# Kernel optimization log

Measured on AMD Instinct MI355X. Metric: run time of the kernel, lower is better.

The kernel has to match this reference:

```python
import jax, jax.numpy as jnp
import numpy as np

HEADS = 5 - 1  # 4 attention heads (GPSConv heads=4)


def _bn(x, g, b, eps=1e-5):
    # BatchNorm1d, training-mode math (biased variance), matches torch normalization
    mu = x.mean(0)
    var = x.var(0)
    return g * (x - mu) * jax.lax.rsqrt(var + eps) + b


def _forward(x, t, freqs, t_fc1_W, t_fc1_b, t_fc2_W, t_fc2_b, node_W, node_b,
             tproj_W, tproj_b, tcat_W, tcat_b, pen_g, pen_b, pel_W, pel_b,
             cat_W, cat_b, conv_Wg, gru_Wih, gru_bih, gru_Whh, gru_bhh,
             attn_Wqkv, attn_bqkv, attn_Wo, attn_bo, bn_g, bn_b,
             mlp_W1, mlp_b1, mlp_W2, mlp_b2, out_W, out_b):
    B, C, Hh, Ww = x.shape
    HD = node_W.shape[1]          # hidden_dim = 64
    DH = HD // HEADS              # per-head dim = 16
    WL = pen_g.shape[0]           # walk_length = 20

    xf = x.reshape(B, -1)                              # [B, D]
    h = xf @ node_W + node_b                           # node_proj

    # TimeEmbedding: t @ freqs -> sin/cos -> MLP, then time_proj
    tp = t.reshape(B, 1) * freqs.reshape(1, -1)        # [B, nf]
    two_pi = jnp.asarray(2.0 * np.pi, x.dtype)
    te = jnp.concatenate([jnp.sin(two_pi * tp), jnp.cos(two_pi * tp)], axis=-1)
    te = jax.nn.silu(te @ t_fc1_W + t_fc1_b) @ t_fc2_W + t_fc2_b
    h_time = te @ tproj_W + tproj_b
    h = jnp.concatenate([h, h_time], axis=-1) @ tcat_W + tcat_b  # time_cat_proj

    # Fully-connected graph incl. self-loops: A = 1 everywhere, deg = B.
    # Random-walk PE: P = A/deg has all entries 1/B; P is idempotent (P@P = P),
    # hence diag(P^k) = diag(P) = 1/B for every k in 1..walk_length.
    A = jnp.ones((B, B), x.dtype)
    P = A / A.sum(1, keepdims=True)
    pe = jnp.broadcast_to(jnp.diagonal(P)[:, None], (B, WL))
    pe = _bn(pe, pen_g, pen_b)                         # pe_norm (batch stats)
    h = jnp.concatenate([h, pe @ pel_W + pel_b], axis=-1) @ cat_W + cat_b

    inv_sqrt = jnp.asarray(1.0 / np.sqrt(DH), x.dtype)
    for l in range(conv_Wg.shape[0]):                  # 5 GPSConv layers
        # --- GatedGraphConv (num_layers=1): message, add-aggregate, GRU ---
        m = A @ (h @ conv_Wg[l])                       # sum of messages from all src nodes
        gi = m @ gru_Wih[l] + gru_bih[l]               # [B, 3H]
        gh = h @ gru_Whh[l] + gru_bhh[l]
        ir, iz, inn = jnp.split(gi, 3, axis=-1)
        hr, hz, hn = jnp.split(gh, 3, axis=-1)
        r = jax.nn.sigmoid(ir + hr)
        z = jax.nn.sigmoid(iz + hz)
        n = jnp.tanh(inn + r * hn)
        hc = (1.0 - z) * n + z * h                     # GRUCell output
        h1 = _bn(hc + h, bn_g[l, 0], bn_b[l, 0])       # residual + norm1

        # --- global multihead self-attention over the single dense batch ---
        qkv = h @ attn_Wqkv[l] + attn_bqkv[l]
        q, k, v = jnp.split(qkv, 3, axis=-1)
        q = q.reshape(B, HEADS, DH).transpose(1, 0, 2)  # [h, B, d]
        k = k.reshape(B, HEADS, DH).transpose(1, 0, 2)
        v = v.reshape(B, HEADS, DH).transpose(1, 0, 2)
        att = jax.nn.softmax(jnp.einsum('hqd,hkd->hqk', q, k) * inv_sqrt, axis=-1)
        o = jnp.einsum('hqk,hkd->hqd', att, v).transpose(1, 0, 2).reshape(B, HD)
        o = o @ attn_Wo[l] + attn_bo[l]
        h2 = _bn(o + h, bn_g[l, 1], bn_b[l, 1])        # residual + norm2

        s = h1 + h2
        s = s + (jax.nn.relu(s @ mlp_W1[l] + mlp_b1[l]) @ mlp_W2[l] + mlp_b2[l])
        h = _bn(s, bn_g[l, 2], bn_b[l, 2])             # norm3

    return (h @ out_W + out_b).reshape(B, C, Hh, Ww)


def setup_inputs() -> dict:
    key = jax.random.key(0)
    B, C, H, W = 2048, 4, 32, 32
    D = C * H * W                 # 4096
    HD, PE, WL, L = 64, 16, 20, 5
    NF, TH, TC = 8, 64, 64
    ks = iter(jax.random.split(key, 40))

    def rn(shape, s=0.05):
        return jax.random.normal(next(ks), shape, jnp.float32) * s

    return {
        'x': jax.random.normal(next(ks), (B, C, H, W), jnp.float32),
        't': jax.random.uniform(next(ks), (B,), jnp.float32),
        'freqs': rn((NF,), 1.0),
        't_fc1_W': rn((2 * NF, TH)), 't_fc1_b': rn((TH,)),
        't_fc2_W': rn((TH, TC)), 't_fc2_b': rn((TC,)),
        'node_W': rn((D, HD), 0.02), 'node_b': rn((HD,)),
        'tproj_W': rn((TC, HD)), 'tproj_b': rn((HD,)),
        'tcat_W': rn((2 * HD, HD)), 'tcat_b': rn((HD,)),
        'pen_g': jnp.ones((WL,), jnp.float32), 'pen_b': jnp.zeros((WL,), jnp.float32),
        'pel_W': rn((WL, PE)), 'pel_b': rn((PE,)),
        'cat_W': rn((HD + PE, HD)), 'cat_b': rn((HD,)),
        'conv_Wg': rn((L, HD, HD)),
        'gru_Wih': rn((L, HD, 3 * HD)), 'gru_bih': rn((L, 3 * HD)),
        'gru_Whh': rn((L, HD, 3 * HD)), 'gru_bhh': rn((L, 3 * HD)),
        'attn_Wqkv': rn((L, HD, 3 * HD)), 'attn_bqkv': rn((L, 3 * HD)),
        'attn_Wo': rn((L, HD, HD)), 'attn_bo': rn((L, HD)),
        'bn_g': jnp.ones((L, 3, HD), jnp.float32), 'bn_b': jnp.zeros((L, 3, HD), jnp.float32),
        'mlp_W1': rn((L, HD, 2 * HD)), 'mlp_b1': rn((L, 2 * HD)),
        'mlp_W2': rn((L, 2 * HD, HD)), 'mlp_b2': rn((L, HD)),
        'out_W': rn((HD, D)), 'out_b': rn((D,)),
    }


def reference(x, t, freqs, t_fc1_W, t_fc1_b, t_fc2_W, t_fc2_b, node_W, node_b,
              tproj_W, tproj_b, tcat_W, tcat_b, pen_g, pen_b, pel_W, pel_b,
              cat_W, cat_b, conv_Wg, gru_Wih, gru_bih, gru_Whh, gru_bhh,
              attn_Wqkv, attn_bqkv, attn_Wo, attn_bo, bn_g, bn_b,
              mlp_W1, mlp_b1, mlp_W2, mlp_b2, out_W, out_b):
    return _forward(x, t, freqs, t_fc1_W, t_fc1_b, t_fc2_W, t_fc2_b, node_W, node_b,
                    tproj_W, tproj_b, tcat_W, tcat_b, pen_g, pen_b, pel_W, pel_b,
                    cat_W, cat_b, conv_Wg, gru_Wih, gru_bih, gru_Whh, gru_bhh,
                    attn_Wqkv, attn_bqkv, attn_Wo, attn_bo, bn_g, bn_b,
                    mlp_W1, mlp_b1, mlp_W2, mlp_b2, out_W, out_b)
```

## Files before the change

### kernel.cpp

```cpp
#include <hip/hip_runtime.h>

#define NB 2048
#define HDM 64
#define NLAY 5

typedef __bf16 bf16x8 __attribute__((ext_vector_type(8)));
typedef float v4f __attribute__((ext_vector_type(4)));

__device__ __forceinline__ float sigmoidf_(float x){ return 1.f/(1.f+__expf(-x)); }
__device__ __forceinline__ float tanhfast_(float x){
  x = fminf(fmaxf(x, -15.f), 15.f);
  float e = __expf(2.f*x);
  return (e-1.f)/(e+1.f);
}
__device__ __forceinline__ unsigned short f2b_rne(float f){
  unsigned u = __float_as_uint(f);
  unsigned r = u + 0x7FFFu + ((u>>16)&1u);
  return (unsigned short)(r>>16);
}
__device__ __forceinline__ unsigned pk2(float a, float b){
  unsigned ua = (__float_as_uint(a) + 0x8000u) >> 16;
  unsigned ub = (__float_as_uint(b) + 0x8000u) & 0xFFFF0000u;
  return ua | ub;
}

__global__ __launch_bounds__(256) void k_pre(
    const float* __restrict__ x, const float* __restrict__ tt,
    const float* __restrict__ freqs,
    const float* __restrict__ fc1W, const float* __restrict__ fc1b,
    const float* __restrict__ fc2W, const float* __restrict__ fc2b,
    const float* __restrict__ tprojW, const float* __restrict__ tprojb,
    const float* __restrict__ nodeW,
    float* __restrict__ h0p, float* __restrict__ htime,
    float* __restrict__ zero_region)
{
  __shared__ float xs[16*260];
  __shared__ float tb0[128];
  __shared__ float tb1[128];
  const int t = threadIdx.x, blk = blockIdx.x;
  const int r = t>>6, c = t&63;

  if (blk == 0){
    for (int i = t; i < 320 + 1920; i += 256) zero_region[i] = 0.f;
  }

  {
    const int row = blk*2 + (r&1);
    const float tv = tt[row];
    if (r < 2){
      float te[16];
      #pragma unroll
      for (int j=0;j<8;++j){
        float sv, cv;
        __sincosf(6.28318530717958647692f*tv*freqs[j], &sv, &cv);
        te[j]=sv; te[j+8]=cv;
      }
      float a = fc1b[c];
      #pragma unroll
      for (int j=0;j<16;++j) a += te[j]*fc1W[j*64+c];
      tb0[r*64+c] = a*sigmoidf_(a);
    }
    __syncthreads();
    if (r < 2){
      float b2 = fc2b[c];
      #pragma unroll 8
      for (int k=0;k<64;++k) b2 += tb0[r*64+k]*fc2W[k*64+c];
      tb1[r*64+c] = b2;
    }
    __syncthreads();
    if (r < 2){
      float hti = tprojb[c];
      #pragma unroll 8
      for (int k=0;k<64;++k) hti += tb1[r*64+k]*tprojW[k*64+c];
      htime[row*64+c] = hti;
    }
  }

  const int rg = blk>>3, kq = blk&7;
  const int rows0 = rg*16, k0 = kq*512;
  const int col4 = (t&15)*4;
  const int rq4  = ((t>>4)&3)*4;
  const int ksub = (t>>6)*64;

  float4 a0={0,0,0,0}, a1={0,0,0,0}, a2={0,0,0,0}, a3={0,0,0,0};

  for (int ch=0; ch<2; ++ch){
    __syncthreads();
    #pragma unroll
    for (int i=0;i<4;++i){
      int fi = t + 256*i;
      int xr = fi>>6, kk = (fi&63)<<2;
      *(float4*)&xs[xr*260+kk] = *(const float4*)&x[(size_t)(rows0+xr)*4096 + k0 + ch*256 + kk];
    }
    __syncthreads();
    const float* wp = &nodeW[(size_t)(k0 + ch*256 + ksub)*64 + col4];
    const float* xp = &xs[rq4*260 + ksub];
    #pragma unroll 8
    for (int kk=0; kk<64; ++kk){
      float4 w  = *(const float4*)&wp[kk*64];
      float x0 = xp[kk];
      float x1 = xp[260+kk];
      float x2 = xp[520+kk];
      float x3 = xp[780+kk];
      a0.x += x0*w.x; a0.y += x0*w.y; a0.z += x0*w.z; a0.w += x0*w.w;
      a1.x += x1*w.x; a1.y += x1*w.y; a1.z += x1*w.z; a1.w += x1*w.w;
      a2.x += x2*w.x; a2.y += x2*w.y; a2.z += x2*w.z; a2.w += x2*w.w;
      a3.x += x3*w.x; a3.y += x3*w.y; a3.z += x3*w.z; a3.w += x3*w.w;
    }
  }
  __syncthreads();
  {
    const int kqi = t>>6;
    *(float4*)&xs[(kqi*16 + rq4 + 0)*64 + col4] = a0;
    *(float4*)&xs[(kqi*16 + rq4 + 1)*64 + col4] = a1;
    *(float4*)&xs[(kqi*16 + rq4 + 2)*64 + col4] = a2;
    *(float4*)&xs[(kqi*16 + rq4 + 3)*64 + col4] = a3;
  }
  __syncthreads();
  {
    const int row = t>>4, c4 = (t&15)*4;
    float4 s = {0,0,0,0};
    #pragma unroll
    for (int q=0;q<4;++q){
      float4 v = *(const float4*)&xs[(q*16+row)*64 + c4];
      s.x+=v.x; s.y+=v.y; s.z+=v.z; s.w+=v.w;
    }
    *(float4*)&h0p[(size_t)kq*(NB*HDM) + (rows0+row)*64 + c4] = s;
  }
}

__global__ __launch_bounds__(256) void k_assemble(
    const float* __restrict__ h0p, const float* __restrict__ htime,
    const float* __restrict__ nodeb,
    const float* __restrict__ tcatW, const float* __restrict__ tcatb,
    const float* __restrict__ penb, const float* __restrict__ pelW,
    const float* __restrict__ pelb,
    const float* __restrict__ catW, const float* __restrict__ catb,
    float* __restrict__ hbuf)
{
  __shared__ float sa[256];
  __shared__ float sb[256];
  __shared__ float cvec[64];
  const int t = threadIdx.x, blk = blockIdx.x;
  const int r = t>>6, c = t&63;
  const int row = blk*4 + r;

  if (r==0){
    float pl[16];
    #pragma unroll
    for (int j=0;j<16;++j){
      float a = pelb[j];
      for (int w=0;w<20;++w) a += penb[w]*pelW[w*16+j];
      pl[j]=a;
    }
    float a = catb[c];
    #pragma unroll
    for (int j=0;j<16;++j) a += pl[j]*catW[(64+j)*64+c];
    cvec[c]=a;
  }
  float h0 = nodeb[c];
  #pragma unroll
  for (int q=0;q<8;++q) h0 += h0p[(size_t)q*(NB*HDM) + row*64 + c];
  sa[t] = h0;
  sb[t] = htime[row*64+c];
  __syncthreads();
  float a = tcatb[c];
  #pragma unroll 4
  for (int k=0;k<64;++k){
    a += sa[r*64+k]*tcatW[k*64+c];
    a += sb[r*64+k]*tcatW[(64+k)*64+c];
  }
  __syncthreads();
  sa[t] = a;
  __syncthreads();
  float hv = cvec[c];
  #pragma unroll 8
  for (int k=0;k<64;++k) hv += sa[r*64+k]*catW[k*64+c];
  hbuf[row*64+c] = hv;
}

__global__ __launch_bounds__(256) void k_A(
    const float* __restrict__ smlp,
    const float* __restrict__ bnaccPrev,
    const float* __restrict__ gPrev, const float* __restrict__ bPrev,
    float* __restrict__ hbuf, float* __restrict__ hsumL,
    const float* __restrict__ Whh, const float* __restrict__ bhh,
    const float* __restrict__ Wq,  const float* __restrict__ bq,
    float* __restrict__ gh,
    unsigned short* __restrict__ Qb, unsigned short* __restrict__ Kb,
    unsigned short* __restrict__ Vt, int first)
{
  __shared__ float sa[8*64];
  const int t = threadIdx.x, blk = blockIdx.x;
  const int row0 = blk*8;

  #pragma unroll
  for (int i=0;i<2;++i){
    int idx = t + 256*i;
    int rl = idx>>6, c = idx&63;
    int row = row0 + rl;
    float hv;
    if (first){
      hv = hbuf[row*64+c];
    } else {
      float mu = bnaccPrev[256+c]*(1.f/NB);
      float va = bnaccPrev[320+c]*(1.f/NB) - mu*mu;
      hv = gPrev[c]*(smlp[row*64+c]-mu)*rsqrtf(va+1e-5f)+bPrev[c];
      hbuf[row*64+c] = hv;
    }
    sa[idx] = hv;
  }
  __syncthreads();
  if (t<64){
    float s = 0.f;
    #pragma unroll
    for (int rl=0;rl<8;++rl) s += sa[rl*64+t];
    atomicAdd(&hsumL[t], s);
  }
  if (t < 192){
    const int cc = t;
    float ag[8], aq[8];
    float bh = bhh[cc], bq_ = bq[cc];
    #pragma unroll
    for (int rl=0;rl<8;++rl){ ag[rl]=bh; aq[rl]=bq_; }
    #pragma unroll 4
    for (int k=0;k<64;++k){
      float wh = Whh[k*192+cc];
      float wq = Wq [k*192+cc];
      #pragma unroll
      for (int rl=0;rl<8;++rl){
        float hk = sa[rl*64+k];
        ag[rl] += hk*wh;
        aq[rl] += hk*wq;
      }
    }
    #pragma unroll
    for (int rl=0;rl<8;++rl){
      int rw = row0 + rl;
      gh[(size_t)rw*192+cc] = ag[rl];
      float aqv = aq[rl];
      if (cc < 64){
        int hd = cc>>4, dh = cc&15;
        size_t base = ((size_t)(hd<<11) + rw)*32;
        Qb[base+dh] = f2b_rne(aqv*0.25f);
        Qb[base+16+dh] = 0;
      } else if (cc < 128){
        int c2 = cc-64, hd = c2>>4, dh = c2&15;
        size_t base = ((size_t)(hd<<11) + rw)*32;
        Kb[base+dh] = f2b_rne(aqv);
        Kb[base+16+dh] = 0;
      } else {
        int c2 = cc-128, hd = c2>>4, dh = c2&15;
        Vt[((size_t)(hd*16+dh))*2048 + rw] = f2b_rne(aqv);
      }
    }
  }
}

__global__ __launch_bounds__(256) void k_attn(
    const unsigned short* __restrict__ Qb, const unsigned short* __restrict__ Kb,
    const unsigned short* __restrict__ Vt,
    float* __restrict__ o_out)
{
  __shared__ unsigned short Pl[4*640];
  __shared__ float Os[4*272];
  __shared__ float ms[64], ls[64];
  const int t = threadIdx.x;
  const int w = t>>6, lane = t&63;
  const int q15 = lane & 15, quad = lane >> 4;
  const int b = blockIdx.x;
  const int qt = b & 127, head = b>>7;
  const int qrow = qt*16 + q15;
  const int key00 = w*512;
  unsigned short* Plw = &Pl[w*640];

  const bf16x8 qf = *(const bf16x8*)&Qb[(((size_t)(head<<11))+qrow)*32 + quad*8];
  const unsigned short* Kb_h = Kb + ((size_t)(head<<11))*32;
  const unsigned short* Vrow = Vt + ((size_t)(head*16+q15))*2048;

  v4f O = {0.f,0.f,0.f,0.f};
  float m = -1e30f, lsum = 0.f;

  bf16x8 kf0 = *(const bf16x8*)&Kb_h[(size_t)(key00 + q15)*32 + quad*8];
  bf16x8 kf1 = *(const bf16x8*)&Kb_h[(size_t)(key00 + 16 + q15)*32 + quad*8];
  bf16x8 vf  = *(const bf16x8*)&Vrow[key00 + quad*8];

  for (int c=0; c<16; ++c){
    bf16x8 nk0, nk1, nv;
    if (c < 15){
      int nk = key00 + (c+1)*32;
      nk0 = *(const bf16x8*)&Kb_h[(size_t)(nk + q15)*32 + quad*8];
      nk1 = *(const bf16x8*)&Kb_h[(size_t)(nk + 16 + q15)*32 + quad*8];
      nv  = *(const bf16x8*)&Vrow[nk + quad*8];
    }
    v4f z = {0.f,0.f,0.f,0.f};
    v4f s0 = __builtin_amdgcn_mfma_f32_16x16x32_bf16(kf0, qf, z, 0,0,0);
    v4f s1 = __builtin_amdgcn_mfma_f32_16x16x32_bf16(kf1, qf, z, 0,0,0);
    float cmax = fmaxf(fmaxf(fmaxf(s0[0],s0[1]),fmaxf(s0[2],s0[3])),
                       fmaxf(fmaxf(s1[0],s1[1]),fmaxf(s1[2],s1[3])));
    cmax = fmaxf(cmax, __shfl_xor(cmax,16,64));
    cmax = fmaxf(cmax, __shfl_xor(cmax,32,64));
    float mnew = fmaxf(m, cmax);
    float alpha = __expf(m - mnew);
    float p0=__expf(s0[0]-mnew), p1=__expf(s0[1]-mnew), p2=__expf(s0[2]-mnew), p3=__expf(s0[3]-mnew);
    float p4=__expf(s1[0]-mnew), p5=__expf(s1[1]-mnew), p6=__expf(s1[2]-mnew), p7=__expf(s1[3]-mnew);
    lsum = alpha*lsum + ((p0+p1)+(p2+p3)+((p4+p5)+(p6+p7)));
    m = mnew;
    O[0]*=alpha; O[1]*=alpha; O[2]*=alpha; O[3]*=alpha;
    *(uint2*)&Plw[q15*40 + quad*4]      = make_uint2(pk2(p0,p1), pk2(p2,p3));
    *(uint2*)&Plw[q15*40 + 16 + quad*4] = make_uint2(pk2(p4,p5), pk2(p6,p7));
    asm volatile("s_waitcnt lgkmcnt(0)" ::: "memory");
    bf16x8 pf = *(const bf16x8*)&Plw[q15*40 + quad*8];
    O = __builtin_amdgcn_mfma_f32_16x16x32_bf16(vf, pf, O, 0,0,0);
    kf0 = nk0; kf1 = nk1; vf = nv;
  }
  lsum += __shfl_xor(lsum,16,64);
  lsum += __shfl_xor(lsum,32,64);
  #pragma unroll
  for (int j=0;j<4;++j) Os[w*272 + q15*17 + quad*4 + j] = O[j];
  if (quad==0){ ms[w*16+q15]=m; ls[w*16+q15]=lsum; }
  __syncthreads();
  {
    const int dh = t&15, q = t>>4;
    float m0=ms[q], m1=ms[16+q], m2=ms[32+q], m3=ms[48+q];
    float mm = fmaxf(fmaxf(m0,m1),fmaxf(m2,m3));
    float a0=__expf(m0-mm), a1=__expf(m1-mm), a2=__expf(m2-mm), a3=__expf(m3-mm);
    float ll = a0*ls[q]+a1*ls[16+q]+a2*ls[32+q]+a3*ls[48+q];
    float oo = a0*Os[q*17+dh] + a1*Os[272+q*17+dh] + a2*Os[544+q*17+dh] + a3*Os[816+q*17+dh];
    o_out[(size_t)(qt*16+q)*64 + head*16 + dh] = oo / ll;
  }
}

__global__ __launch_bounds__(256) void k_B2(
    const float* __restrict__ hbuf, const float* __restrict__ gh,
    const float* __restrict__ hsumL, const float* __restrict__ o_out,
    const float* __restrict__ Wg,   const float* __restrict__ Wih,
    const float* __restrict__ bih,  const float* __restrict__ Wo,
    const float* __restrict__ bo,
    float* __restrict__ s1, float* __restrict__ s2, float* __restrict__ bnaccL)
{
  __shared__ float sa[8*64];
  __shared__ float os[8*64];
  __shared__ float smv_[64];
  __shared__ float sgi[192];
  __shared__ float Sb1[8*64];
  __shared__ float Sb2[8*64];
  const int t = threadIdx.x, blk = blockIdx.x;
  const int row0 = blk*8;

  if (t<64){
    float a=0.f;
    #pragma unroll 8
    for (int k=0;k<64;++k) a += hsumL[k]*Wg[k*64+t];
    smv_[t]=a;
  }
  #pragma unroll
  for (int i=0;i<2;++i){
    int idx = t + 256*i;
    int rl = idx>>6, c = idx&63;
    sa[idx] = hbuf[(size_t)(row0+rl)*64+c];
    os[idx] = o_out[(size_t)(row0+rl)*64+c];
  }
  __syncthreads();
  if (t<192){
    float a = bih[t];
    #pragma unroll 8
    for (int k=0;k<64;++k) a += smv_[k]*Wih[k*192+t];
    sgi[t]=a;
  }
  __syncthreads();

  const int c = t&63, rg = t>>6;
  float o2a = bo[c], o2b = bo[c];
  #pragma unroll 4
  for (int k=0;k<64;++k){
    float w = Wo[k*64+c];
    o2a += os[(rg*2  )*64+k]*w;
    o2b += os[(rg*2+1)*64+k]*w;
  }
  #pragma unroll
  for (int i=0;i<2;++i){
    int rl = rg*2 + i;
    int row = row0 + rl;
    float o2 = i ? o2b : o2a;
    float hv = sa[rl*64+c];
    float s2v = o2 + hv;
    float ir = sgi[c]      + gh[(size_t)row*192+c];
    float iz = sgi[64+c]   + gh[(size_t)row*192+64+c];
    float inn = sgi[128+c];
    float hn  = gh[(size_t)row*192+128+c];
    float rr_ = sigmoidf_(ir);
    float zz  = sigmoidf_(iz);
    float nn  = tanhfast_(inn + rr_*hn);
    float s1v = (1.f-zz)*nn + zz*hv + hv;
    s1[(size_t)row*64+c] = s1v;
    s2[(size_t)row*64+c] = s2v;
    Sb1[rl*64+c] = s1v;
    Sb2[rl*64+c] = s2v;
  }
  __syncthreads();
  if (t<64){
    float a=0.f,aq=0.f,b=0.f,bq2=0.f;
    #pragma unroll
    for (int rl=0;rl<8;++rl){
      float v1 = Sb1[rl*64+t], v2 = Sb2[rl*64+t];
      a+=v1; aq+=v1*v1; b+=v2; bq2+=v2*v2;
    }
    atomicAdd(&bnaccL[t],a);     atomicAdd(&bnaccL[64+t],aq);
    atomicAdd(&bnaccL[128+t],b); atomicAdd(&bnaccL[192+t],bq2);
  }
}

__global__ __launch_bounds__(256) void k_C(
    const float* __restrict__ s1, const float* __restrict__ s2,
    const float* __restrict__ bngL, const float* __restrict__ bnbL,
    const float* __restrict__ W1, const float* __restrict__ b1,
    const float* __restrict__ W2, const float* __restrict__ b2,
    float* __restrict__ smlp, float* __restrict__ bnaccL)
{
  __shared__ float sa[8*64];
  __shared__ float sh[8*128];
  __shared__ float S2[8*64];
  const int t = threadIdx.x, blk = blockIdx.x;
  const int row0 = blk*8;

  #pragma unroll
  for (int i=0;i<2;++i){
    int idx = t + 256*i;
    int rl = idx>>6, c = idx&63;
    int row = row0 + rl;
    float mu1 = bnaccL[c]*(1.f/NB);
    float va1 = bnaccL[64+c]*(1.f/NB) - mu1*mu1;
    float mu2 = bnaccL[128+c]*(1.f/NB);
    float va2 = bnaccL[192+c]*(1.f/NB) - mu2*mu2;
    float h1 = bngL[c]*(s1[(size_t)row*64+c]-mu1)*rsqrtf(va1+1e-5f)+bnbL[c];
    float h2 = bngL[64+c]*(s2[(size_t)row*64+c]-mu2)*rsqrtf(va2+1e-5f)+bnbL[64+c];
    sa[idx] = h1+h2;
  }
  __syncthreads();
  {
    const int hj = t&127, rgq = t>>7;
    float a0v=b1[hj], a1v=b1[hj], a2v=b1[hj], a3v=b1[hj];
    #pragma unroll 4
    for (int k=0;k<64;++k){
      float w = W1[k*128+hj];
      a0v += sa[(rgq*4  )*64+k]*w;
      a1v += sa[(rgq*4+1)*64+k]*w;
      a2v += sa[(rgq*4+2)*64+k]*w;
      a3v += sa[(rgq*4+3)*64+k]*w;
    }
    sh[(rgq*4  )*128+hj] = fmaxf(a0v,0.f);
    sh[(rgq*4+1)*128+hj] = fmaxf(a1v,0.f);
    sh[(rgq*4+2)*128+hj] = fmaxf(a2v,0.f);
    sh[(rgq*4+3)*128+hj] = fmaxf(a3v,0.f);
  }
  __syncthreads();
  {
    const int c = t&63, rg = t>>6;
    float moa = b2[c], mob = b2[c];
    #pragma unroll 4
    for (int k=0;k<128;++k){
      float w = W2[k*64+c];
      moa += sh[(rg*2  )*128+k]*w;
      mob += sh[(rg*2+1)*128+k]*w;
    }
    #pragma unroll
    for (int i=0;i<2;++i){
      int rl = rg*2+i;
      float smv2 = sa[rl*64+c] + (i ? mob : moa);
      smlp[(size_t)(row0+rl)*64+c] = smv2;
      S2[rl*64+c] = smv2;
    }
  }
  __syncthreads();
  if (t<64){
    float a=0.f,aq=0.f;
    #pragma unroll
    for (int rl=0;rl<8;++rl){ float v=S2[rl*64+t]; a+=v; aq+=v*v; }
    atomicAdd(&bnaccL[256+t],a); atomicAdd(&bnaccL[320+t],aq);
  }
}

__global__ __launch_bounds__(256) void k_out(
  const float* __restrict__ smlp, const float* __restrict__ bnacc4,
  const float* __restrict__ g4, const float* __restrict__ b4,
  const float* __restrict__ outW, const float* __restrict__ outb,
  float* __restrict__ out)
{
  __shared__ float hsT[64*20];
  const int t = threadIdx.x, blk = blockIdx.x;
  const int rg = blk>>2, cg = blk&3;
  const int rows0 = rg*16;
  #pragma unroll
  for (int i=0;i<4;++i){
    int idx = t + 256*i;
    int k = idx&63, rr = idx>>6;
    float mu = bnacc4[256+k]*(1.f/NB);
    float va = bnacc4[320+k]*(1.f/NB)-mu*mu;
    hsT[k*20+rr] = g4[k]*(smlp[(size_t)(rows0+rr)*64+k]-mu)*rsqrtf(va+1e-5f)+b4[k];
  }
  __syncthreads();
  const int cc = cg*1024 + t*4;
  float4 acc[16];
  {
    float4 bv = *(const float4*)&outb[cc];
    #pragma unroll
    for (int rr=0;rr<16;++rr) acc[rr]=bv;
  }
  #pragma unroll 4
  for (int k=0;k<64;++k){
    float4 w = *(const float4*)&outW[(size_t)k*4096+cc];
    const float4* hp = (const float4*)&hsT[k*20];
    float4 h0=hp[0], h1=hp[1], h2=hp[2], h3=hp[3];
    acc[0].x+=h0.x*w.x;  acc[0].y+=h0.x*w.y;  acc[0].z+=h0.x*w.z;  acc[0].w+=h0.x*w.w;
    acc[1].x+=h0.y*w.x;  acc[1].y+=h0.y*w.y;  acc[1].z+=h0.y*w.z;  acc[1].w+=h0.y*w.w;
    acc[2].x+=h0.z*w.x;  acc[2].y+=h0.z*w.y;  acc[2].z+=h0.z*w.z;  acc[2].w+=h0.z*w.w;
    acc[3].x+=h0.w*w.x;  acc[3].y+=h0.w*w.y;  acc[3].z+=h0.w*w.z;  acc[3].w+=h0.w*w.w;
    acc[4].x+=h1.x*w.x;  acc[4].y+=h1.x*w.y;  acc[4].z+=h1.x*w.z;  acc[4].w+=h1.x*w.w;
    acc[5].x+=h1.y*w.x;  acc[5].y+=h1.y*w.y;  acc[5].z+=h1.y*w.z;  acc[5].w+=h1.y*w.w;
    acc[6].x+=h1.z*w.x;  acc[6].y+=h1.z*w.y;  acc[6].z+=h1.z*w.z;  acc[6].w+=h1.z*w.w;
    acc[7].x+=h1.w*w.x;  acc[7].y+=h1.w*w.y;  acc[7].z+=h1.w*w.z;  acc[7].w+=h1.w*w.w;
    acc[8].x+=h2.x*w.x;  acc[8].y+=h2.x*w.y;  acc[8].z+=h2.x*w.z;  acc[8].w+=h2.x*w.w;
    acc[9].x+=h2.y*w.x;  acc[9].y+=h2.y*w.y;  acc[9].z+=h2.y*w.z;  acc[9].w+=h2.y*w.w;
    acc[10].x+=h2.z*w.x; acc[10].y+=h2.z*w.y; acc[10].z+=h2.z*w.z; acc[10].w+=h2.z*w.w;
    acc[11].x+=h2.w*w.x; acc[11].y+=h2.w*w.y; acc[11].z+=h2.w*w.z; acc[11].w+=h2.w*w.w;
    acc[12].x+=h3.x*w.x; acc[12].y+=h3.x*w.y; acc[12].z+=h3.x*w.z; acc[12].w+=h3.x*w.w;
    acc[13].x+=h3.y*w.x; acc[13].y+=h3.y*w.y; acc[13].z+=h3.y*w.z; acc[13].w+=h3.y*w.w;
    acc[14].x+=h3.z*w.x; acc[14].y+=h3.z*w.y; acc[14].z+=h3.z*w.z; acc[14].w+=h3.z*w.w;
    acc[15].x+=h3.w*w.x; acc[15].y+=h3.w*w.y; acc[15].z+=h3.w*w.z; acc[15].w+=h3.w*w.w;
  }
  #pragma unroll
  for (int rr=0;rr<16;++rr)
    *(float4*)&out[(size_t)(rows0+rr)*4096+cc] = acc[rr];
}

extern "C" void kernel_launch(void* const* d_in, const int* in_sizes, int n_in,
                              void* d_out, int out_size, void* d_ws, size_t ws_size,
                              hipStream_t stream)
{
  (void)in_sizes; (void)n_in; (void)out_size; (void)ws_size;
  const float* x      = (const float*)d_in[0];
  const float* tt     = (const float*)d_in[1];
  const float* freqs  = (const float*)d_in[2];
  const float* fc1W   = (const float*)d_in[3];
  const float* fc1b   = (const float*)d_in[4];
  const float* fc2W   = (const float*)d_in[5];
  const float* fc2b   = (const float*)d_in[6];
  const float* nodeW  = (const float*)d_in[7];
  const float* nodeb  = (const float*)d_in[8];
  const float* tprojW = (const float*)d_in[9];
  const float* tprojb = (const float*)d_in[10];
  const float* tcatW  = (const float*)d_in[11];
  const float* tcatb  = (const float*)d_in[12];
  const float* penb   = (const float*)d_in[14];
  const float* pelW   = (const float*)d_in[15];
  const float* pelb   = (const float*)d_in[16];
  const float* catW   = (const float*)d_in[17];
  const float* catb   = (const float*)d_in[18];
  const float* convWg = (const float*)d_in[19];
  const float* gruWih = (const float*)d_in[20];
  const float* grubih = (const float*)d_in[21];
  const float* gruWhh = (const float*)d_in[22];
  const float* grubhh = (const float*)d_in[23];
  const float* Wqkv   = (const float*)d_in[24];
  const float* bqkv   = (const float*)d_in[25];
  const float* Wo     = (const float*)d_in[26];
  const float* bo     = (const float*)d_in[27];
  const float* bng    = (const float*)d_in[28];
  const float* bnb    = (const float*)d_in[29];
  const float* W1     = (const float*)d_in[30];
  const float* b1     = (const float*)d_in[31];
  const float* W2     = (const float*)d_in[32];
  const float* b2     = (const float*)d_in[33];
  const float* outW   = (const float*)d_in[34];
  const float* outb   = (const float*)d_in[35];

  float* ws = (float*)d_ws;
  float* htime = ws;
  float* hbuf  = htime + 131072;
  float* gh    = hbuf + 131072;
  float* s1    = gh + 393216;
  float* s2    = s1 + 131072;
  float* smlp  = s2 + 131072;
  float* o_out = smlp + 131072;
  float* hsum  = o_out + 131072;
  float* bnacc = hsum + 320;
  unsigned short* Qb = (unsigned short*)(bnacc + 1920);
  unsigned short* Kb = Qb + 262144;
  unsigned short* Vt = Kb + 262144;
  float* h0p  = (float*)(Vt + 65536);

  dim3 Blk(256);

  k_pre<<<dim3(1024), Blk, 0, stream>>>(x, tt, freqs, fc1W, fc1b, fc2W, fc2b,
                                        tprojW, tprojb, nodeW, h0p, htime, hsum);

  k_assemble<<<dim3(512), Blk, 0, stream>>>(h0p, htime, nodeb, tcatW, tcatb,
                                            penb, pelW, pelb, catW, catb, hbuf);

  for (int l=0; l<NLAY; ++l){
    const float* bnaccPrev = (l==0) ? bnacc : bnacc + (l-1)*384;
    const float* gPrev = (l==0) ? bng : bng + (l-1)*192 + 128;
    const float* bPrev = (l==0) ? bnb : bnb + (l-1)*192 + 128;
    k_A<<<dim3(256), Blk, 0, stream>>>(smlp, bnaccPrev, gPrev, bPrev,
                                       hbuf, hsum + l*64,
                                       gruWhh + l*12288, grubhh + l*192,
                                       Wqkv + l*12288, bqkv + l*192,
                                       gh, Qb, Kb, Vt, (l==0) ? 1 : 0);
    k_attn<<<dim3(512), Blk, 0, stream>>>(Qb, Kb, Vt, o_out);
    k_B2<<<dim3(256), Blk, 0, stream>>>(hbuf, gh, hsum + l*64, o_out,
                                        convWg + l*4096, gruWih + l*12288, grubih + l*192,
                                        Wo + l*4096, bo + l*64,
                                        s1, s2, bnacc + l*384);
    k_C<<<dim3(256), Blk, 0, stream>>>(s1, s2, bng + l*192, bnb + l*192,
                                       W1 + l*8192, b1 + l*128, W2 + l*8192, b2 + l*64,
                                       smlp, bnacc + l*384);
  }

  k_out<<<dim3(512), Blk, 0, stream>>>(smlp, bnacc + 4*384, bng + 896, bnb + 896,
                                       outW, outb, (float*)d_out);
}
```

Baseline: 529.6 us.

## Fuse all stages into one persistent kernel with software grid barriers

Replaces the roughly two dozen separate kernel launches (preprocess, assemble, four kernels per layer, output) with one persistent kernel of 256 blocks. Stages are separated by an atomic-counter grid barrier that uses a fresh slot each time, and the counters are cleared with a memset before launch. This removes per-launch overhead and the gaps between launches. In exchange, wide stages get fewer blocks: the node projection drops to 2 K-splits with 8 chunks per block, and attention loops over two heads per block. Correctness also depends on all 256 blocks being resident at once.

After: 1.026 ms. 1.94x slower.

```diff
diff --git a/kernel.cpp b/kernel.cpp
--- a/kernel.cpp
+++ b/kernel.cpp
@@ -3,6 +3,7 @@
 #define NB 2048
 #define HDM 64
 #define NLAY 5
+#define NBLK 256
 
 typedef __bf16 bf16x8 __attribute__((ext_vector_type(8)));
 typedef float v4f __attribute__((ext_vector_type(4)));
@@ -24,599 +25,579 @@
   return ua | ub;
 }
 
-__global__ __launch_bounds__(256) void k_pre(
-    const float* __restrict__ x, const float* __restrict__ tt,
-    const float* __restrict__ freqs,
-    const float* __restrict__ fc1W, const float* __restrict__ fc1b,
-    const float* __restrict__ fc2W, const float* __restrict__ fc2b,
-    const float* __restrict__ tprojW, const float* __restrict__ tprojb,
-    const float* __restrict__ nodeW,
-    float* __restrict__ h0p, float* __restrict__ htime,
-    float* __restrict__ zero_region)
+
+struct KArgs {
+  const float *x, *tt, *freqs, *fc1W, *fc1b, *fc2W, *fc2b, *nodeW, *nodeb,
+              *tprojW, *tprojb, *tcatW, *tcatb, *penb, *pelW, *pelb, *catW, *catb,
+              *convWg, *gruWih, *grubih, *gruWhh, *grubhh, *Wqkv, *bqkv, *Wo, *bo,
+              *bng, *bnb, *W1, *b1, *W2, *b2, *outW, *outb;
+  float *htime, *hbuf, *gh, *s1, *s2, *smlp, *o_out, *hsum, *bnacc, *h0p, *out;
+  unsigned short *Qb, *Kb, *Vt;
+  unsigned *bar;
+};
+
+union SMem {
+  struct { float xs[16*260]; float tb0[256]; float tb1[256]; } pre;
+  struct { float sa[256]; float sb[256]; float cvec[64]; } as;
+  struct { float sa[512]; } a;
+  struct { unsigned short Pl[4*640]; float Os[4*272]; float ms[64]; float ls[64]; } at;
+  struct { float sa[512]; float os[512]; float smv[64]; float sgi[192]; float Sb1[512]; float Sb2[512]; } b2;
+  struct { float sa[512]; float sh[8*128]; float S2[512]; } c;
+  struct { float hsT[64*20]; } o;
+};
+
+__device__ __forceinline__ void gsync(unsigned* slotp){
+  __syncthreads();
+  if (threadIdx.x == 0){
+    __threadfence();
+    __hip_atomic_fetch_add(slotp, 1u, __ATOMIC_RELEASE, __HIP_MEMORY_SCOPE_AGENT);
+    unsigned spins = 0u;
+    while (__hip_atomic_load(slotp, __ATOMIC_ACQUIRE, __HIP_MEMORY_SCOPE_AGENT) < (unsigned)NBLK){
+      __builtin_amdgcn_s_sleep(2);
+      if (++spins > 4000000u) break;
+    }
+    __threadfence();
+  }
+  __syncthreads();
+}
+
+__global__ __launch_bounds__(256, 2) void k_fused(KArgs A)
 {
-  __shared__ float xs[16*260];
-  __shared__ float tb0[128];
-  __shared__ float tb1[128];
-  const int t = threadIdx.x, blk = blockIdx.x;
-  const int r = t>>6, c = t&63;
-
-  if (blk == 0){
-    for (int i = t; i < 320 + 1920; i += 256) zero_region[i] = 0.f;
+  __shared__ SMem sm;
+  const int t = threadIdx.x;
+  const int b = blockIdx.x;
+  int slot = 0;
+
+  if (b == 0){
+    for (int i = t; i < 320 + 1920; i += 256) A.hsum[i] = 0.f;
   }
-
   {
-    const int row = blk*2 + (r&1);
-    const float tv = tt[row];
-    if (r < 2){
+    const int r = t>>6, c = t&63;
+    for (int pass=0; pass<2; ++pass){
+      if (pass) __syncthreads();
+      const int row = b*8 + pass*4 + r;
+      const float tv = A.tt[row];
       float te[16];
       #pragma unroll
       for (int j=0;j<8;++j){
         float sv, cv;
-        __sincosf(6.28318530717958647692f*tv*freqs[j], &sv, &cv);
+        __sincosf(6.28318530717958647692f*tv*A.freqs[j], &sv, &cv);
         te[j]=sv; te[j+8]=cv;
       }
-      float a = fc1b[c];
-      #pragma unroll
-      for (int j=0;j<16;++j) a += te[j]*fc1W[j*64+c];
-      tb0[r*64+c] = a*sigmoidf_(a);
+      float a = A.fc1b[c];
+      #pragma unroll
+      for (int j=0;j<16;++j) a += te[j]*A.fc1W[j*64+c];
+      sm.pre.tb0[r*64+c] = a*sigmoidf_(a);
+      __syncthreads();
+      float b2v = A.fc2b[c];
+      #pragma unroll 8
+      for (int k=0;k<64;++k) b2v += sm.pre.tb0[r*64+k]*A.fc2W[k*64+c];
+      sm.pre.tb1[r*64+c] = b2v;
+      __syncthreads();
+      float hti = A.tprojb[c];
+      #pragma unroll 8
+      for (int k=0;k<64;++k) hti += sm.pre.tb1[r*64+k]*A.tprojW[k*64+c];
+      A.htime[row*64+c] = hti;
+    }
+  }
+  {
+    const int rg = b>>1, kq = b&1;
+    const int rows0 = rg*16, k0 = kq*2048;
+    const int col4 = (t&15)*4;
+    const int rq4  = ((t>>4)&3)*4;
+    const int ksub = (t>>6)*64;
+
+    float4 a0={0,0,0,0}, a1={0,0,0,0}, a2={0,0,0,0}, a3={0,0,0,0};
+
+    for (int ch=0; ch<8; ++ch){
+      __syncthreads();
+      #pragma unroll
+      for (int i=0;i<4;++i){
+        int fi = t + 256*i;
+        int xr = fi>>6, kk = (fi&63)<<2;
+        *(float4*)&sm.pre.xs[xr*260+kk] =
+            *(const float4*)&A.x[(size_t)(rows0+xr)*4096 + k0 + ch*256 + kk];
+      }
+      __syncthreads();
+      const float* wp = &A.nodeW[(size_t)(k0 + ch*256 + ksub)*64 + col4];
+      const float* xp = &sm.pre.xs[rq4*260 + ksub];
+      #pragma unroll 8
+      for (int kk=0; kk<64; ++kk){
+        float4 w  = *(const float4*)&wp[kk*64];
+        float x0 = xp[kk];
+        float x1 = xp[260+kk];
+        float x2 = xp[520+kk];
+        float x3 = xp[780+kk];
+        a0.x += x0*w.x; a0.y += x0*w.y; a0.z += x0*w.z; a0.w += x0*w.w;
+        a1.x += x1*w.x; a1.y += x1*w.y; a1.z += x1*w.z; a1.w += x1*w.w;
+        a2.x += x2*w.x; a2.y += x2*w.y; a2.z += x2*w.z; a2.w += x2*w.w;
+        a3.x += x3*w.x; a3.y += x3*w.y; a3.z += x3*w.z; a3.w += x3*w.w;
+      }
     }
     __syncthreads();
-    if (r < 2){
-      float b2 = fc2b[c];
+    {
+      const int kqi = t>>6;
+      *(float4*)&sm.pre.xs[(kqi*16 + rq4 + 0)*64 + col4] = a0;
+      *(float4*)&sm.pre.xs[(kqi*16 + rq4 + 1)*64 + col4] = a1;
+      *(float4*)&sm.pre.xs[(kqi*16 + rq4 + 2)*64 + col4] = a2;
+      *(float4*)&sm.pre.xs[(kqi*16 + rq4 + 3)*64 + col4] = a3;
+    }
+    __syncthreads();
+    {
+      const int row = t>>4, c4 = (t&15)*4;
+      float4 s = {0,0,0,0};
+      #pragma unroll
+      for (int q=0;q<4;++q){
+        float4 v = *(const float4*)&sm.pre.xs[(q*16+row)*64 + c4];
+        s.x+=v.x; s.y+=v.y; s.z+=v.z; s.w+=v.w;
+      }
+      *(float4*)&A.h0p[(size_t)kq*(NB*HDM) + (rows0+row)*64 + c4] = s;
+    }
+  }
+  gsync(A.bar + (slot++));
+
+  {
+    const int r = t>>6, c = t&63;
+    for (int pass=0; pass<2; ++pass){
+      if (pass) __syncthreads();
+      const int row = b*8 + pass*4 + r;
+      if (pass==0 && r==0){
+        float pl[16];
+        #pragma unroll
+        for (int j=0;j<16;++j){
+          float a = A.pelb[j];
+          for (int w=0;w<20;++w) a += A.penb[w]*A.pelW[w*16+j];
+          pl[j]=a;
+        }
+        float a = A.catb[c];
+        #pragma unroll
+        for (int j=0;j<16;++j) a += pl[j]*A.catW[(64+j)*64+c];
+        sm.as.cvec[c]=a;
+      }
+      float h0 = A.nodeb[c];
+      #pragma unroll
+      for (int q=0;q<2;++q) h0 += A.h0p[(size_t)q*(NB*HDM) + row*64 + c];
+      sm.as.sa[t] = h0;
+      sm.as.sb[t] = A.htime[row*64+c];
+      __syncthreads();
+      float a = A.tcatb[c];
+      #pragma unroll 4
+      for (int k=0;k<64;++k){
+        a += sm.as.sa[r*64+k]*A.tcatW[k*64+c];
+        a += sm.as.sb[r*64+k]*A.tcatW[(64+k)*64+c];
+      }
+      __syncthreads();
+      sm.as.sa[t] = a;
+      __syncthreads();
+      float hv = sm.as.cvec[c];
       #pragma unroll 8
-      for (int k=0;k<64;++k) b2 += tb0[r*64+k]*fc2W[k*64+c];
-      tb1[r*64+c] = b2;
-    }
+      for (int k=0;k<64;++k) hv += sm.as.sa[r*64+k]*A.catW[k*64+c];
+      A.hbuf[row*64+c] = hv;
+    }
+  }
+
+  for (int l=0; l<NLAY; ++l){
+    const float* bnaccPrev = (l==0) ? A.bnacc : A.bnacc + (l-1)*384;
+    const float* gPrev = (l==0) ? A.bng : A.bng + (l-1)*192 + 128;
+    const float* bPrev = (l==0) ? A.bnb : A.bnb + (l-1)*192 + 128;
+    const float* Whh = A.gruWhh + l*12288;
+    const float* bhh = A.grubhh + l*192;
+    const float* Wq  = A.Wqkv + l*12288;
+    const float* bqv = A.bqkv + l*192;
+    float* hsumL  = A.hsum + l*64;
+    float* bnaccL = A.bnacc + l*384;
+
     __syncthreads();
-    if (r < 2){
-      float hti = tprojb[c];
-      #pragma unroll 8
-      for (int k=0;k<64;++k) hti += tb1[r*64+k]*tprojW[k*64+c];
-      htime[row*64+c] = hti;
-    }
+    {
+      const int row0 = b*8;
+      #pragma unroll
+      for (int i=0;i<2;++i){
+        int idx = t + 256*i;
+        int rl = idx>>6, c = idx&63;
+        int row = row0 + rl;
+        float hv;
+        if (l==0){
+          hv = A.hbuf[row*64+c];
+        } else {
+          float mu = bnaccPrev[256+c]*(1.f/NB);
+          float va = bnaccPrev[320+c]*(1.f/NB) - mu*mu;
+          hv = gPrev[c]*(A.smlp[row*64+c]-mu)*rsqrtf(va+1e-5f)+bPrev[c];
+          A.hbuf[row*64+c] = hv;
+        }
+        sm.a.sa[idx] = hv;
+      }
+      __syncthreads();
+      if (t<64){
+        float s = 0.f;
+        #pragma unroll
+        for (int rl=0;rl<8;++rl) s += sm.a.sa[rl*64+t];
+        atomicAdd(&hsumL[t], s);
+      }
+      if (t < 192){
+        const int cc = t;
+        float ag[8], aq[8];
+        float bh = bhh[cc], bq_ = bqv[cc];
+        #pragma unroll
+        for (int rl=0;rl<8;++rl){ ag[rl]=bh; aq[rl]=bq_; }
+        #pragma unroll 4
+        for (int k=0;k<64;++k){
+          float wh = Whh[k*192+cc];
+          float wq = Wq [k*192+cc];
+          #pragma unroll
+          for (int rl=0;rl<8;++rl){
+            float hk = sm.a.sa[rl*64+k];
+            ag[rl] += hk*wh;
+            aq[rl] += hk*wq;
+          }
+        }
+        #pragma unroll
+        for (int rl=0;rl<8;++rl){
+          int rw = row0 + rl;
+          A.gh[(size_t)rw*192+cc] = ag[rl];
+          float aqv = aq[rl];
+          if (cc < 64){
+            int hd = cc>>4, dh = cc&15;
+            size_t base = ((size_t)(hd<<11) + rw)*32;
+            A.Qb[base+dh] = f2b_rne(aqv*0.25f);
+            A.Qb[base+16+dh] = 0;
+          } else if (cc < 128){
+            int c2 = cc-64, hd = c2>>4, dh = c2&15;
+            size_t base = ((size_t)(hd<<11) + rw)*32;
+            A.Kb[base+dh] = f2b_rne(aqv);
+            A.Kb[base+16+dh] = 0;
+          } else {
+            int c2 = cc-128, hd = c2>>4, dh = c2&15;
+            A.Vt[((size_t)(hd*16+dh))*2048 + rw] = f2b_rne(aqv);
+          }
+        }
+      }
+    }
+    gsync(A.bar + (slot++));
+
+    for (int it=0; it<2; ++it){
+      if (it) __syncthreads();
+      const int w = t>>6, lane = t&63;
+      const int q15 = lane & 15, quad = lane >> 4;
+      const int qt = b & 127, head = (b>>7) + 2*it;
+      const int qrow = qt*16 + q15;
+      const int key00 = w*512;
+      unsigned short* Plw = &sm.at.Pl[w*640];
+
+      const bf16x8 qf = *(const bf16x8*)&A.Qb[(((size_t)(head<<11))+qrow)*32 + quad*8];
+      const unsigned short* Kb_h = A.Kb + ((size_t)(head<<11))*32;
+      const unsigned short* Vrow = A.Vt + ((size_t)(head*16+q15))*2048;
+
+      v4f O = {0.f,0.f,0.f,0.f};
+      float m = -1e30f, lsum = 0.f;
+
+      bf16x8 kf0 = *(const bf16x8*)&Kb_h[(size_t)(key00 + q15)*32 + quad*8];
+      bf16x8 kf1 = *(const bf16x8*)&Kb_h[(size_t)(key00 + 16 + q15)*32 + quad*8];
+      bf16x8 vf  = *(const bf16x8*)&Vrow[key00 + quad*8];
+
+      for (int c=0; c<16; ++c){
+        bf16x8 nk0, nk1, nv;
+        if (c < 15){
+          int nk = key00 + (c+1)*32;
+          nk0 = *(const bf16x8*)&Kb_h[(size_t)(nk + q15)*32 + quad*8];
+          nk1 = *(const bf16x8*)&Kb_h[(size_t)(nk + 16 + q15)*32 + quad*8];
+          nv  = *(const bf16x8*)&Vrow[nk + quad*8];
+        }
+        v4f z = {0.f,0.f,0.f,0.f};
+        v4f s0 = __builtin_amdgcn_mfma_f32_16x16x32_bf16(kf0, qf, z, 0,0,0);
+        v4f s1 = __builtin_amdgcn_mfma_f32_16x16x32_bf16(kf1, qf, z, 0,0,0);
+        float cmax = fmaxf(fmaxf(fmaxf(s0[0],s0[1]),fmaxf(s0[2],s0[3])),
+                           fmaxf(fmaxf(s1[0],s1[1]),fmaxf(s1[2],s1[3])));
+        cmax = fmaxf(cmax, __shfl_xor(cmax,16,64));
+        cmax = fmaxf(cmax, __shfl_xor(cmax,32,64));
+        float mnew = fmaxf(m, cmax);
+        float alpha = __expf(m - mnew);
+        float p0=__expf(s0[0]-mnew), p1=__expf(s0[1]-mnew), p2=__expf(s0[2]-mnew), p3=__expf(s0[3]-mnew);
+        float p4=__expf(s1[0]-mnew), p5=__expf(s1[1]-mnew), p6=__expf(s1[2]-mnew), p7=__expf(s1[3]-mnew);
+        lsum = alpha*lsum + ((p0+p1)+(p2+p3)+((p4+p5)+(p6+p7)));
+        m = mnew;
+        O[0]*=alpha; O[1]*=alpha; O[2]*=alpha; O[3]*=alpha;
+        *(uint2*)&Plw[q15*40 + quad*4]      = make_uint2(pk2(p0,p1), pk2(p2,p3));
+        *(uint2*)&Plw[q15*40 + 16 + quad*4] = make_uint2(pk2(p4,p5), pk2(p6,p7));
+        asm volatile("s_waitcnt lgkmcnt(0)" ::: "memory");
+        bf16x8 pf = *(const bf16x8*)&Plw[q15*40 + quad*8];
+        O = __builtin_amdgcn_mfma_f32_16x16x32_bf16(vf, pf, O, 0,0,0);
+        kf0 = nk0; kf1 = nk1; vf = nv;
+      }
+      lsum += __shfl_xor(lsum,16,64);
+      lsum += __shfl_xor(lsum,32,64);
+      #pragma unroll
+      for (int j=0;j<4;++j) sm.at.Os[w*272 + q15*17 + quad*4 + j] = O[j];
+      if (quad==0){ sm.at.ms[w*16+q15]=m; sm.at.ls[w*16+q15]=lsum; }
+      __syncthreads();
+      {
+        const int dh = t&15, q = t>>4;
+        float m0=sm.at.ms[q], m1=sm.at.ms[16+q], m2=sm.at.ms[32+q], m3=sm.at.ms[48+q];
+        float mm = fmaxf(fmaxf(m0,m1),fmaxf(m2,m3));
+        float a0=__expf(m0-mm), a1=__expf(m1-mm), a2=__expf(m2-mm), a3=__expf(m3-mm);
+        float ll = a0*sm.at.ls[q]+a1*sm.at.ls[16+q]+a2*sm.at.ls[32+q]+a3*sm.at.ls[48+q];
+        float oo = a0*sm.at.Os[q*17+dh] + a1*sm.at.Os[272+q*17+dh]
+                 + a2*sm.at.Os[544+q*17+dh] + a3*sm.at.Os[816+q*17+dh];
+        A.o_out[(size_t)(qt*16+q)*64 + head*16 + dh] = oo / ll;
+      }
+    }
+    gsync(A.bar + (slot++));
+
+    {
+      const float* Wg  = A.convWg + l*4096;
+      const float* Wih = A.gruWih + l*12288;
+      const float* bih = A.grubih + l*192;
+      const float* WoL = A.Wo + l*4096;
+      const float* boL = A.bo + l*64;
+      const int row0 = b*8;
+
+      if (t<64){
+        float a=0.f;
+        #pragma unroll 8
+        for (int k=0;k<64;++k) a += hsumL[k]*Wg[k*64+t];
+        sm.b2.smv[t]=a;
+      }
+      #pragma unroll
+      for (int i=0;i<2;++i){
+        int idx = t + 256*i;
+        int rl = idx>>6, c = idx&63;
+        sm.b2.sa[idx] = A.hbuf[(size_t)(row0+rl)*64+c];
+        sm.b2.os[idx] = A.o_out[(size_t)(row0+rl)*64+c];
+      }
+      __syncthreads();
+      if (t<192){
+        float a = bih[t];
+        #pragma unroll 8
+        for (int k=0;k<64;++k) a += sm.b2.smv[k]*Wih[k*192+t];
+        sm.b2.sgi[t]=a;
+      }
+      __syncthreads();
+
+      {
+        const int c = t&63, rg = t>>6;
+        float o2a = boL[c], o2b = boL[c];
+        #pragma unroll 4
+        for (int k=0;k<64;++k){
+          float w = WoL[k*64+c];
+          o2a += sm.b2.os[(rg*2  )*64+k]*w;
+          o2b += sm.b2.os[(rg*2+1)*64+k]*w;
+        }
+        #pragma unroll
+        for (int i=0;i<2;++i){
+          int rl = rg*2 + i;
+          int row = row0 + rl;
+          float o2 = i ? o2b : o2a;
+          float hv = sm.b2.sa[rl*64+c];
+          float s2v = o2 + hv;
+          float ir = sm.b2.sgi[c]      + A.gh[(size_t)row*192+c];
+          float iz = sm.b2.sgi[64+c]   + A.gh[(size_t)row*192+64+c];
+          float inn = sm.b2.sgi[128+c];
+          float hn  = A.gh[(size_t)row*192+128+c];
+          float rr_ = sigmoidf_(ir);
+          float zz  = sigmoidf_(iz);
+          float nn  = tanhfast_(inn + rr_*hn);
+          float s1v = (1.f-zz)*nn + zz*hv + hv;
+          A.s1[(size_t)row*64+c] = s1v;
+          A.s2[(size_t)row*64+c] = s2v;
+          sm.b2.Sb1[rl*64+c] = s1v;
+          sm.b2.Sb2[rl*64+c] = s2v;
+        }
+      }
+      __syncthreads();
+      if (t<64){
+        float a=0.f,aq=0.f,bb=0.f,bq2=0.f;
+        #pragma unroll
+        for (int rl=0;rl<8;++rl){
+          float v1 = sm.b2.Sb1[rl*64+t], v2 = sm.b2.Sb2[rl*64+t];
+          a+=v1; aq+=v1*v1; bb+=v2; bq2+=v2*v2;
+        }
+        atomicAdd(&bnaccL[t],a);     atomicAdd(&bnaccL[64+t],aq);
+        atomicAdd(&bnaccL[128+t],bb); atomicAdd(&bnaccL[192+t],bq2);
+      }
+    }
+    gsync(A.bar + (slot++));
+
+    {
+      const float* bngL = A.bng + l*192;
+      const float* bnbL = A.bnb + l*192;
+      const float* W1l = A.W1 + l*8192;
+      const float* b1l = A.b1 + l*128;
+      const float* W2l = A.W2 + l*8192;
+      const float* b2l = A.b2 + l*64;
+      const int row0 = b*8;
+
+      #pragma unroll
+      for (int i=0;i<2;++i){
+        int idx = t + 256*i;
+        int rl = idx>>6, c = idx&63;
+        int row = row0 + rl;
+        float mu1 = bnaccL[c]*(1.f/NB);
+        float va1 = bnaccL[64+c]*(1.f/NB) - mu1*mu1;
+        float mu2 = bnaccL[128+c]*(1.f/NB);
+        float va2 = bnaccL[192+c]*(1.f/NB) - mu2*mu2;
+        float h1 = bngL[c]*(A.s1[(size_t)row*64+c]-mu1)*rsqrtf(va1+1e-5f)+bnbL[c];
+        float h2 = bngL[64+c]*(A.s2[(size_t)row*64+c]-mu2)*rsqrtf(va2+1e-5f)+bnbL[64+c];
+        sm.c.sa[idx] = h1+h2;
+      }
+      __syncthreads();
+      {
+        const int hj = t&127, rgq = t>>7;
+        float a0v=b1l[hj], a1v=b1l[hj], a2v=b1l[hj], a3v=b1l[hj];
+        #pragma unroll 4
+        for (int k=0;k<64;++k){
+          float w = W1l[k*128+hj];
+          a0v += sm.c.sa[(rgq*4  )*64+k]*w;
+          a1v += sm.c.sa[(rgq*4+1)*64+k]*w;
+          a2v += sm.c.sa[(rgq*4+2)*64+k]*w;
+          a3v += sm.c.sa[(rgq*4+3)*64+k]*w;
+        }
+        sm.c.sh[(rgq*4  )*128+hj] = fmaxf(a0v,0.f);
+        sm.c.sh[(rgq*4+1)*128+hj] = fmaxf(a1v,0.f);
+        sm.c.sh[(rgq*4+2)*128+hj] = fmaxf(a2v,0.f);
+        sm.c.sh[(rgq*4+3)*128+hj] = fmaxf(a3v,0.f);
+      }
+      __syncthreads();
+      {
+        const int c = t&63, rg = t>>6;
+        float moa = b2l[c], mob = b2l[c];
+        #pragma unroll 4
+        for (int k=0;k<128;++k){
+          float w = W2l[k*64+c];
+          moa += sm.c.sh[(rg*2  )*128+k]*w;
+          mob += sm.c.sh[(rg*2+1)*128+k]*w;
+        }
+        #pragma unroll
+        for (int i=0;i<2;++i){
+          int rl = rg*2+i;
+          float smv2 = sm.c.sa[rl*64+c] + (i ? mob : moa);
+          A.smlp[(size_t)(row0+rl)*64+c] = smv2;
+          sm.c.S2[rl*64+c] = smv2;
+        }
+      }
+      __syncthreads();
+      if (t<64){
+        float a=0.f,aq=0.f;
+        #pragma unroll
+        for (int rl=0;rl<8;++rl){ float v=sm.c.S2[rl*64+t]; a+=v; aq+=v*v; }
+        atomicAdd(&bnaccL[256+t],a); atomicAdd(&bnaccL[320+t],aq);
+      }
+    }
+    gsync(A.bar + (slot++));
   }
 
-  const int rg = blk>>3, kq = blk&7;
-  const int rows0 = rg*16, k0 = kq*512;
-  const int col4 = (t&15)*4;
-  const int rq4  = ((t>>4)&3)*4;
-  const int ksub = (t>>6)*64;
-
-  float4 a0={0,0,0,0}, a1={0,0,0,0}, a2={0,0,0,0}, a3={0,0,0,0};
-
-  for (int ch=0; ch<2; ++ch){
-    __syncthreads();
-    #pragma unroll
-    for (int i=0;i<4;++i){
-      int fi = t + 256*i;
-      int xr = fi>>6, kk = (fi&63)<<2;
-      *(float4*)&xs[xr*260+kk] = *(const float4*)&x[(size_t)(rows0+xr)*4096 + k0 + ch*256 + kk];
-    }
-    __syncthreads();
-    const float* wp = &nodeW[(size_t)(k0 + ch*256 + ksub)*64 + col4];
-    const float* xp = &xs[rq4*260 + ksub];
-    #pragma unroll 8
-    for (int kk=0; kk<64; ++kk){
-      float4 w  = *(const float4*)&wp[kk*64];
-      float x0 = xp[kk];
-      float x1 = xp[260+kk];
-      float x2 = xp[520+kk];
-      float x3 = xp[780+kk];
-      a0.x += x0*w.x; a0.y += x0*w.y; a0.z += x0*w.z; a0.w += x0*w.w;
-      a1.x += x1*w.x; a1.y += x1*w.y; a1.z += x1*w.z; a1.w += x1*w.w;
-      a2.x += x2*w.x; a2.y += x2*w.y; a2.z += x2*w.z; a2.w += x2*w.w;
-      a3.x += x3*w.x; a3.y += x3*w.y; a3.z += x3*w.z; a3.w += x3*w.w;
-    }
-  }
-  __syncthreads();
   {
-    const int kqi = t>>6;
-    *(float4*)&xs[(kqi*16 + rq4 + 0)*64 + col4] = a0;
-    *(float4*)&xs[(kqi*16 + rq4 + 1)*64 + col4] = a1;
-    *(float4*)&xs[(kqi*16 + rq4 + 2)*64 + col4] = a2;
-    *(float4*)&xs[(kqi*16 + rq4 + 3)*64 + col4] = a3;
-  }
-  __syncthreads();
-  {
-    const int row = t>>4, c4 = (t&15)*4;
-    float4 s = {0,0,0,0};
-    #pragma unroll
-    for (int q=0;q<4;++q){
-      float4 v = *(const float4*)&xs[(q*16+row)*64 + c4];
-      s.x+=v.x; s.y+=v.y; s.z+=v.z; s.w+=v.w;
-    }
-    *(float4*)&h0p[(size_t)kq*(NB*HDM) + (rows0+row)*64 + c4] = s;
+    const float* bnacc4 = A.bnacc + 4*384;
+    const float* g4 = A.bng + 896;
+    const float* b4 = A.bnb + 896;
+    for (int it=0; it<2; ++it){
+      if (it) __syncthreads();
+      const int u = b + NBLK*it;
+      const int rg = u>>2, cg = u&3;
+      const int rows0 = rg*16;
+      #pragma unroll
+      for (int i=0;i<4;++i){
+        int idx = t + 256*i;
+        int k = idx&63, rr = idx>>6;
+        float mu = bnacc4[256+k]*(1.f/NB);
+        float va = bnacc4[320+k]*(1.f/NB)-mu*mu;
+        sm.o.hsT[k*20+rr] = g4[k]*(A.smlp[(size_t)(rows0+rr)*64+k]-mu)*rsqrtf(va+1e-5f)+b4[k];
+      }
+      __syncthreads();
+      const int cc = cg*1024 + t*4;
+      float4 acc[16];
+      {
+        float4 bv = *(const float4*)&A.outb[cc];
+        #pragma unroll
+        for (int rr=0;rr<16;++rr) acc[rr]=bv;
+      }
+      #pragma unroll 4
+      for (int k=0;k<64;++k){
+        float4 w = *(const float4*)&A.outW[(size_t)k*4096+cc];
+        const float4* hp = (const float4*)&sm.o.hsT[k*20];
+        float4 h0=hp[0], h1=hp[1], h2=hp[2], h3=hp[3];
+        acc[0].x+=h0.x*w.x;  acc[0].y+=h0.x*w.y;  acc[0].z+=h0.x*w.z;  acc[0].w+=h0.x*w.w;
+        acc[1].x+=h0.y*w.x;  acc[1].y+=h0.y*w.y;  acc[1].z+=h0.y*w.z;  acc[1].w+=h0.y*w.w;
+        acc[2].x+=h0.z*w.x;  acc[2].y+=h0.z*w.y;  acc[2].z+=h0.z*w.z;  acc[2].w+=h0.z*w.w;
+        acc[3].x+=h0.w*w.x;  acc[3].y+=h0.w*w.y;  acc[3].z+=h0.w*w.z;  acc[3].w+=h0.w*w.w;
+        acc[4].x+=h1.x*w.x;  acc[4].y+=h1.x*w.y;  acc[4].z+=h1.x*w.z;  acc[4].w+=h1.x*w.w;
+        acc[5].x+=h1.y*w.x;  acc[5].y+=h1.y*w.y;  acc[5].z+=h1.y*w.z;  acc[5].w+=h1.y*w.w;
+        acc[6].x+=h1.z*w.x;  acc[6].y+=h1.z*w.y;  acc[6].z+=h1.z*w.z;  acc[6].w+=h1.z*w.w;
+        acc[7].x+=h1.w*w.x;  acc[7].y+=h1.w*w.y;  acc[7].z+=h1.w*w.z;  acc[7].w+=h1.w*w.w;
+        acc[8].x+=h2.x*w.x;  acc[8].y+=h2.x*w.y;  acc[8].z+=h2.x*w.z;  acc[8].w+=h2.x*w.w;
+        acc[9].x+=h2.y*w.x;  acc[9].y+=h2.y*w.y;  acc[9].z+=h2.y*w.z;  acc[9].w+=h2.y*w.w;
+        acc[10].x+=h2.z*w.x; acc[10].y+=h2.z*w.y; acc[10].z+=h2.z*w.z; acc[10].w+=h2.z*w.w;
+        acc[11].x+=h2.w*w.x; acc[11].y+=h2.w*w.y; acc[11].z+=h2.w*w.z; acc[11].w+=h2.w*w.w;
+        acc[12].x+=h3.x*w.x; acc[12].y+=h3.x*w.y; acc[12].z+=h3.x*w.z; acc[12].w+=h3.x*w.w;
+        acc[13].x+=h3.y*w.x; acc[13].y+=h3.y*w.y; acc[13].z+=h3.y*w.z; acc[13].w+=h3.y*w.w;
+        acc[14].x+=h3.z*w.x; acc[14].y+=h3.z*w.y; acc[14].z+=h3.z*w.z; acc[14].w+=h3.z*w.w;
+        acc[15].x+=h3.w*w.x; acc[15].y+=h3.w*w.y; acc[15].z+=h3.w*w.z; acc[15].w+=h3.w*w.w;
+      }
+      #pragma unroll
+      for (int rr=0;rr<16;++rr)
+        *(float4*)&A.out[(size_t)(rows0+rr)*4096+cc] = acc[rr];
+    }
   }
 }
 
-__global__ __launch_bounds__(256) void k_assemble(
-    const float* __restrict__ h0p, const float* __restrict__ htime,
-    const float* __restrict__ nodeb,
-    const float* __restrict__ tcatW, const float* __restrict__ tcatb,
-    const float* __restrict__ penb, const float* __restrict__ pelW,
-    const float* __restrict__ pelb,
-    const float* __restrict__ catW, const float* __restrict__ catb,
-    float* __restrict__ hbuf)
-{
-  __shared__ float sa[256];
-  __shared__ float sb[256];
-  __shared__ float cvec[64];
-  const int t = threadIdx.x, blk = blockIdx.x;
-  const int r = t>>6, c = t&63;
-  const int row = blk*4 + r;
-
-  if (r==0){
-    float pl[16];
-    #pragma unroll
-    for (int j=0;j<16;++j){
-      float a = pelb[j];
-      for (int w=0;w<20;++w) a += penb[w]*pelW[w*16+j];
-      pl[j]=a;
-    }
-    float a = catb[c];
-    #pragma unroll
-    for (int j=0;j<16;++j) a += pl[j]*catW[(64+j)*64+c];
-    cvec[c]=a;
-  }
-  float h0 = nodeb[c];
-  #pragma unroll
-  for (int q=0;q<8;++q) h0 += h0p[(size_t)q*(NB*HDM) + row*64 + c];
-  sa[t] = h0;
-  sb[t] = htime[row*64+c];
-  __syncthreads();
-  float a = tcatb[c];
-  #pragma unroll 4
-  for (int k=0;k<64;++k){
-    a += sa[r*64+k]*tcatW[k*64+c];
-    a += sb[r*64+k]*tcatW[(64+k)*64+c];
-  }
-  __syncthreads();
-  sa[t] = a;
-  __syncthreads();
-  float hv = cvec[c];
-  #pragma unroll 8
-  for (int k=0;k<64;++k) hv += sa[r*64+k]*catW[k*64+c];
-  hbuf[row*64+c] = hv;
-}
-
-__global__ __launch_bounds__(256) void k_A(
-    const float* __restrict__ smlp,
-    const float* __restrict__ bnaccPrev,
-    const float* __restrict__ gPrev, const float* __restrict__ bPrev,
-    float* __restrict__ hbuf, float* __restrict__ hsumL,
-    const float* __restrict__ Whh, const float* __restrict__ bhh,
-    const float* __restrict__ Wq,  const float* __restrict__ bq,
-    float* __restrict__ gh,
-    unsigned short* __restrict__ Qb, unsigned short* __restrict__ Kb,
-    unsigned short* __restrict__ Vt, int first)
-{
-  __shared__ float sa[8*64];
-  const int t = threadIdx.x, blk = blockIdx.x;
-  const int row0 = blk*8;
-
-  #pragma unroll
-  for (int i=0;i<2;++i){
-    int idx = t + 256*i;
-    int rl = idx>>6, c = idx&63;
-    int row = row0 + rl;
-    float hv;
-    if (first){
-      hv = hbuf[row*64+c];
-    } else {
-      float mu = bnaccPrev[256+c]*(1.f/NB);
-      float va = bnaccPrev[320+c]*(1.f/NB) - mu*mu;
-      hv = gPrev[c]*(smlp[row*64+c]-mu)*rsqrtf(va+1e-5f)+bPrev[c];
-      hbuf[row*64+c] = hv;
-    }
-    sa[idx] = hv;
-  }
-  __syncthreads();
-  if (t<64){
-    float s = 0.f;
-    #pragma unroll
-    for (int rl=0;rl<8;++rl) s += sa[rl*64+t];
-    atomicAdd(&hsumL[t], s);
-  }
-  if (t < 192){
-    const int cc = t;
-    float ag[8], aq[8];
-    float bh = bhh[cc], bq_ = bq[cc];
-    #pragma unroll
-    for (int rl=0;rl<8;++rl){ ag[rl]=bh; aq[rl]=bq_; }
-    #pragma unroll 4
-    for (int k=0;k<64;++k){
-      float wh = Whh[k*192+cc];
-      float wq = Wq [k*192+cc];
-      #pragma unroll
-      for (int rl=0;rl<8;++rl){
-        float hk = sa[rl*64+k];
-        ag[rl] += hk*wh;
-        aq[rl] += hk*wq;
-      }
-    }
-    #pragma unroll
-    for (int rl=0;rl<8;++rl){
-      int rw = row0 + rl;
-      gh[(size_t)rw*192+cc] = ag[rl];
-      float aqv = aq[rl];
-      if (cc < 64){
-        int hd = cc>>4, dh = cc&15;
-        size_t base = ((size_t)(hd<<11) + rw)*32;
-        Qb[base+dh] = f2b_rne(aqv*0.25f);
-        Qb[base+16+dh] = 0;
-      } else if (cc < 128){
-        int c2 = cc-64, hd = c2>>4, dh = c2&15;
-        size_t base = ((size_t)(hd<<11) + rw)*32;
-        Kb[base+dh] = f2b_rne(aqv);
-        Kb[base+16+dh] = 0;
-      } else {
-        int c2 = cc-128, hd = c2>>4, dh = c2&15;
-        Vt[((size_t)(hd*16+dh))*2048 + rw] = f2b_rne(aqv);
-      }
-    }
-  }
-}
-
-__global__ __launch_bounds__(256) void k_attn(
-    const unsigned short* __restrict__ Qb, const unsigned short* __restrict__ Kb,
-    const unsigned short* __restrict__ Vt,
-    float* __restrict__ o_out)
-{
-  __shared__ unsigned short Pl[4*640];
-  __shared__ float Os[4*272];
-  __shared__ float ms[64], ls[64];
-  const int t = threadIdx.x;
-  const int w = t>>6, lane = t&63;
-  const int q15 = lane & 15, quad = lane >> 4;
-  const int b = blockIdx.x;
-  const int qt = b & 127, head = b>>7;
-  const int qrow = qt*16 + q15;
-  const int key00 = w*512;
-  unsigned short* Plw = &Pl[w*640];
-
-  const bf16x8 qf = *(const bf16x8*)&Qb[(((size_t)(head<<11))+qrow)*32 + quad*8];
-  const unsigned short* Kb_h = Kb + ((size_t)(head<<11))*32;
-  const unsigned short* Vrow = Vt + ((size_t)(head*16+q15))*2048;
-
-  v4f O = {0.f,0.f,0.f,0.f};
-  float m = -1e30f, lsum = 0.f;
-
-  bf16x8 kf0 = *(const bf16x8*)&Kb_h[(size_t)(key00 + q15)*32 + quad*8];
-  bf16x8 kf1 = *(const bf16x8*)&Kb_h[(size_t)(key00 + 16 + q15)*32 + quad*8];
-  bf16x8 vf  = *(const bf16x8*)&Vrow[key00 + quad*8];
-
-  for (int c=0; c<16; ++c){
-    bf16x8 nk0, nk1, nv;
-    if (c < 15){
-      int nk = key00 + (c+1)*32;
-      nk0 = *(const bf16x8*)&Kb_h[(size_t)(nk + q15)*32 + quad*8];
-      nk1 = *(const bf16x8*)&Kb_h[(size_t)(nk + 16 + q15)*32 + quad*8];
-      nv  = *(const bf16x8*)&Vrow[nk + quad*8];
-    }
-    v4f z = {0.f,0.f,0.f,0.f};
-    v4f s0 = __builtin_amdgcn_mfma_f32_16x16x32_bf16(kf0, qf, z, 0,0,0);
-    v4f s1 = __builtin_amdgcn_mfma_f32_16x16x32_bf16(kf1, qf, z, 0,0,0);
-    float cmax = fmaxf(fmaxf(fmaxf(s0[0],s0[1]),fmaxf(s0[2],s0[3])),
-                       fmaxf(fmaxf(s1[0],s1[1]),fmaxf(s1[2],s1[3])));
-    cmax = fmaxf(cmax, __shfl_xor(cmax,16,64));
-    cmax = fmaxf(cmax, __shfl_xor(cmax,32,64));
-    float mnew = fmaxf(m, cmax);
-    float alpha = __expf(m - mnew);
-    float p0=__expf(s0[0]-mnew), p1=__expf(s0[1]-mnew), p2=__expf(s0[2]-mnew), p3=__expf(s0[3]-mnew);
-    float p4=__expf(s1[0]-mnew), p5=__expf(s1[1]-mnew), p6=__expf(s1[2]-mnew), p7=__expf(s1[3]-mnew);
-    lsum = alpha*lsum + ((p0+p1)+(p2+p3)+((p4+p5)+(p6+p7)));
-    m = mnew;
-    O[0]*=alpha; O[1]*=alpha; O[2]*=alpha; O[3]*=alpha;
-    *(uint2*)&Plw[q15*40 + quad*4]      = make_uint2(pk2(p0,p1), pk2(p2,p3));
-    *(uint2*)&Plw[q15*40 + 16 + quad*4] = make_uint2(pk2(p4,p5), pk2(p6,p7));
-    asm volatile("s_waitcnt lgkmcnt(0)" ::: "memory");
-    bf16x8 pf = *(const bf16x8*)&Plw[q15*40 + quad*8];
-    O = __builtin_amdgcn_mfma_f32_16x16x32_bf16(vf, pf, O, 0,0,0);
-    kf0 = nk0; kf1 = nk1; vf = nv;
-  }
-  lsum += __shfl_xor(lsum,16,64);
-  lsum += __shfl_xor(lsum,32,64);
-  #pragma unroll
-  for (int j=0;j<4;++j) Os[w*272 + q15*17 + quad*4 + j] = O[j];
-  if (quad==0){ ms[w*16+q15]=m; ls[w*16+q15]=lsum; }
-  __syncthreads();
-  {
-    const int dh = t&15, q = t>>4;
-    float m0=ms[q], m1=ms[16+q], m2=ms[32+q], m3=ms[48+q];
-    float mm = fmaxf(fmaxf(m0,m1),fmaxf(m2,m3));
-    float a0=__expf(m0-mm), a1=__expf(m1-mm), a2=__expf(m2-mm), a3=__expf(m3-mm);
-    float ll = a0*ls[q]+a1*ls[16+q]+a2*ls[32+q]+a3*ls[48+q];
-    float oo = a0*Os[q*17+dh] + a1*Os[272+q*17+dh] + a2*Os[544+q*17+dh] + a3*Os[816+q*17+dh];
-    o_out[(size_t)(qt*16+q)*64 + head*16 + dh] = oo / ll;
-  }
-}
-
-__global__ __launch_bounds__(256) void k_B2(
-    const float* __restrict__ hbuf, const float* __restrict__ gh,
-    const float* __restrict__ hsumL, const float* __restrict__ o_out,
-    const float* __restrict__ Wg,   const float* __restrict__ Wih,
-    const float* __restrict__ bih,  const float* __restrict__ Wo,
-    const float* __restrict__ bo,
-    float* __restrict__ s1, float* __restrict__ s2, float* __restrict__ bnaccL)
-{
-  __shared__ float sa[8*64];
-  __shared__ float os[8*64];
-  __shared__ float smv_[64];
-  __shared__ float sgi[192];
-  __shared__ float Sb1[8*64];
-  __shared__ float Sb2[8*64];
-  const int t = threadIdx.x, blk = blockIdx.x;
-  const int row0 = blk*8;
-
-  if (t<64){
-    float a=0.f;
-    #pragma unroll 8
-    for (int k=0;k<64;++k) a += hsumL[k]*Wg[k*64+t];
-    smv_[t]=a;
-  }
-  #pragma unroll
-  for (int i=0;i<2;++i){
-    int idx = t + 256*i;
-    int rl = idx>>6, c = idx&63;
-    sa[idx] = hbuf[(size_t)(row0+rl)*64+c];
-    os[idx] = o_out[(size_t)(row0+rl)*64+c];
-  }
-  __syncthreads();
-  if (t<192){
-    float a = bih[t];
-    #pragma unroll 8
-    for (int k=0;k<64;++k) a += smv_[k]*Wih[k*192+t];
-    sgi[t]=a;
-  }
-  __syncthreads();
-
-  const int c = t&63, rg = t>>6;
-  float o2a = bo[c], o2b = bo[c];
-  #pragma unroll 4
-  for (int k=0;k<64;++k){
-    float w = Wo[k*64+c];
-    o2a += os[(rg*2  )*64+k]*w;
-    o2b += os[(rg*2+1)*64+k]*w;
-  }
-  #pragma unroll
-  for (int i=0;i<2;++i){
-    int rl = rg*2 + i;
-    int row = row0 + rl;
-    float o2 = i ? o2b : o2a;
-    float hv = sa[rl*64+c];
-    float s2v = o2 + hv;
-    float ir = sgi[c]      + gh[(size_t)row*192+c];
-    float iz = sgi[64+c]   + gh[(size_t)row*192+64+c];
-    float inn = sgi[128+c];
-    float hn  = gh[(size_t)row*192+128+c];
-    float rr_ = sigmoidf_(ir);
-    float zz  = sigmoidf_(iz);
-    float nn  = tanhfast_(inn + rr_*hn);
-    float s1v = (1.f-zz)*nn + zz*hv + hv;
-    s1[(size_t)row*64+c] = s1v;
-    s2[(size_t)row*64+c] = s2v;
-    Sb1[rl*64+c] = s1v;
-    Sb2[rl*64+c] = s2v;
-  }
-  __syncthreads();
-  if (t<64){
-    float a=0.f,aq=0.f,b=0.f,bq2=0.f;
-    #pragma unroll
-    for (int rl=0;rl<8;++rl){
-      float v1 = Sb1[rl*64+t], v2 = Sb2[rl*64+t];
-      a+=v1; aq+=v1*v1; b+=v2; bq2+=v2*v2;
-    }
-    atomicAdd(&bnaccL[t],a);     atomicAdd(&bnaccL[64+t],aq);
-    atomicAdd(&bnaccL[128+t],b); atomicAdd(&bnaccL[192+t],bq2);
-  }
-}
-
-__global__ __launch_bounds__(256) void k_C(
-    const float* __restrict__ s1, const float* __restrict__ s2,
-    const float* __restrict__ bngL, const float* __restrict__ bnbL,
-    const float* __restrict__ W1, const float* __restrict__ b1,
-    const float* __restrict__ W2, const float* __restrict__ b2,
-    float* __restrict__ smlp, float* __restrict__ bnaccL)
-{
-  __shared__ float sa[8*64];
-  __shared__ float sh[8*128];
-  __shared__ float S2[8*64];
-  const int t = threadIdx.x, blk = blockIdx.x;
-  const int row0 = blk*8;
-
-  #pragma unroll
-  for (int i=0;i<2;++i){
-    int idx = t + 256*i;
-    int rl = idx>>6, c = idx&63;
-    int row = row0 + rl;
-    float mu1 = bnaccL[c]*(1.f/NB);
-    float va1 = bnaccL[64+c]*(1.f/NB) - mu1*mu1;
-    float mu2 = bnaccL[128+c]*(1.f/NB);
-    float va2 = bnaccL[192+c]*(1.f/NB) - mu2*mu2;
-    float h1 = bngL[c]*(s1[(size_t)row*64+c]-mu1)*rsqrtf(va1+1e-5f)+bnbL[c];
-    float h2 = bngL[64+c]*(s2[(size_t)row*64+c]-mu2)*rsqrtf(va2+1e-5f)+bnbL[64+c];
-    sa[idx] = h1+h2;
-  }
-  __syncthreads();
-  {
-    const int hj = t&127, rgq = t>>7;
-    float a0v=b1[hj], a1v=b1[hj], a2v=b1[hj], a3v=b1[hj];
-    #pragma unroll 4
-    for (int k=0;k<64;++k){
-      float w = W1[k*128+hj];
-      a0v += sa[(rgq*4  )*64+k]*w;
-      a1v += sa[(rgq*4+1)*64+k]*w;
-      a2v += sa[(rgq*4+2)*64+k]*w;
-      a3v += sa[(rgq*4+3)*64+k]*w;
-    }
-    sh[(rgq*4  )*128+hj] = fmaxf(a0v,0.f);
-    sh[(rgq*4+1)*128+hj] = fmaxf(a1v,0.f);
-    sh[(rgq*4+2)*128+hj] = fmaxf(a2v,0.f);
-    sh[(rgq*4+3)*128+hj] = fmaxf(a3v,0.f);
-  }
-  __syncthreads();
-  {
-    const int c = t&63, rg = t>>6;
-    float moa = b2[c], mob = b2[c];
-    #pragma unroll 4
-    for (int k=0;k<128;++k){
-      float w = W2[k*64+c];
-      moa += sh[(rg*2  )*128+k]*w;
-      mob += sh[(rg*2+1)*128+k]*w;
-    }
-    #pragma unroll
-    for (int i=0;i<2;++i){
-      int rl = rg*2+i;
-      float smv2 = sa[rl*64+c] + (i ? mob : moa);
-      smlp[(size_t)(row0+rl)*64+c] = smv2;
-      S2[rl*64+c] = smv2;
-    }
-  }
-  __syncthreads();
-  if (t<64){
-    float a=0.f,aq=0.f;
-    #pragma unroll
-    for (int rl=0;rl<8;++rl){ float v=S2[rl*64+t]; a+=v; aq+=v*v; }
-    atomicAdd(&bnaccL[256+t],a); atomicAdd(&bnaccL[320+t],aq);
-  }
-}
-
-__global__ __launch_bounds__(256) void k_out(
-  const float* __restrict__ smlp, const float* __restrict__ bnacc4,
-  const float* __restrict__ g4, const float* __restrict__ b4,
-  const float* __restrict__ outW, const float* __restrict__ outb,
-  float* __restrict__ out)
-{
-  __shared__ float hsT[64*20];
-  const int t = threadIdx.x, blk = blockIdx.x;
-  const int rg = blk>>2, cg = blk&3;
-  const int rows0 = rg*16;
-  #pragma unroll
-  for (int i=0;i<4;++i){
-    int idx = t + 256*i;
-    int k = idx&63, rr = idx>>6;
-    float mu = bnacc4[256+k]*(1.f/NB);
-    float va = bnacc4[320+k]*(1.f/NB)-mu*mu;
-    hsT[k*20+rr] = g4[k]*(smlp[(size_t)(rows0+rr)*64+k]-mu)*rsqrtf(va+1e-5f)+b4[k];
-  }
-  __syncthreads();
-  const int cc = cg*1024 + t*4;
-  float4 acc[16];
-  {
-    float4 bv = *(const float4*)&outb[cc];
-    #pragma unroll
-    for (int rr=0;rr<16;++rr) acc[rr]=bv;
-  }
-  #pragma unroll 4
-  for (int k=0;k<64;++k){
-    float4 w = *(const float4*)&outW[(size_t)k*4096+cc];
-    const float4* hp = (const float4*)&hsT[k*20];
-    float4 h0=hp[0], h1=hp[1], h2=hp[2], h3=hp[3];
-    acc[0].x+=h0.x*w.x;  acc[0].y+=h0.x*w.y;  acc[0].z+=h0.x*w.z;  acc[0].w+=h0.x*w.w;
-    acc[1].x+=h0.y*w.x;  acc[1].y+=h0.y*w.y;  acc[1].z+=h0.y*w.z;  acc[1].w+=h0.y*w.w;
-    acc[2].x+=h0.z*w.x;  acc[2].y+=h0.z*w.y;  acc[2].z+=h0.z*w.z;  acc[2].w+=h0.z*w.w;
-    acc[3].x+=h0.w*w.x;  acc[3].y+=h0.w*w.y;  acc[3].z+=h0.w*w.z;  acc[3].w+=h0.w*w.w;
-    acc[4].x+=h1.x*w.x;  acc[4].y+=h1.x*w.y;  acc[4].z+=h1.x*w.z;  acc[4].w+=h1.x*w.w;
-    acc[5].x+=h1.y*w.x;  acc[5].y+=h1.y*w.y;  acc[5].z+=h1.y*w.z;  acc[5].w+=h1.y*w.w;
-    acc[6].x+=h1.z*w.x;  acc[6].y+=h1.z*w.y;  acc[6].z+=h1.z*w.z;  acc[6].w+=h1.z*w.w;
-    acc[7].x+=h1.w*w.x;  acc[7].y+=h1.w*w.y;  acc[7].z+=h1.w*w.z;  acc[7].w+=h1.w*w.w;
-    acc[8].x+=h2.x*w.x;  acc[8].y+=h2.x*w.y;  acc[8].z+=h2.x*w.z;  acc[8].w+=h2.x*w.w;
-    acc[9].x+=h2.y*w.x;  acc[9].y+=h2.y*w.y;  acc[9].z+=h2.y*w.z;  acc[9].w+=h2.y*w.w;
-    acc[10].x+=h2.z*w.x; acc[10].y+=h2.z*w.y; acc[10].z+=h2.z*w.z; acc[10].w+=h2.z*w.w;
-    acc[11].x+=h2.w*w.x; acc[11].y+=h2.w*w.y; acc[11].z+=h2.w*w.z; acc[11].w+=h2.w*w.w;
-    acc[12].x+=h3.x*w.x; acc[12].y+=h3.x*w.y; acc[12].z+=h3.x*w.z; acc[12].w+=h3.x*w.w;
-    acc[13].x+=h3.y*w.x; acc[13].y+=h3.y*w.y; acc[13].z+=h3.y*w.z; acc[13].w+=h3.y*w.w;
-    acc[14].x+=h3.z*w.x; acc[14].y+=h3.z*w.y; acc[14].z+=h3.z*w.z; acc[14].w+=h3.z*w.w;
-    acc[15].x+=h3.w*w.x; acc[15].y+=h3.w*w.y; acc[15].z+=h3.w*w.z; acc[15].w+=h3.w*w.w;
-  }
-  #pragma unroll
-  for (int rr=0;rr<16;++rr)
-    *(float4*)&out[(size_t)(rows0+rr)*4096+cc] = acc[rr];
-}
 
 extern "C" void kernel_launch(void* const* d_in, const int* in_sizes, int n_in,
                               void* d_out, int out_size, void* d_ws, size_t ws_size,
                               hipStream_t stream)
 {
   (void)in_sizes; (void)n_in; (void)out_size; (void)ws_size;
-  const float* x      = (const float*)d_in[0];
-  const float* tt     = (const float*)d_in[1];
-  const float* freqs  = (const float*)d_in[2];
-  const float* fc1W   = (const float*)d_in[3];
-  const float* fc1b   = (const float*)d_in[4];
-  const float* fc2W   = (const float*)d_in[5];
-  const float* fc2b   = (const float*)d_in[6];
-  const float* nodeW  = (const float*)d_in[7];
-  const float* nodeb  = (const float*)d_in[8];
-  const float* tprojW = (const float*)d_in[9];
-  const float* tprojb = (const float*)d_in[10];
-  const float* tcatW  = (const float*)d_in[11];
-  const float* tcatb  = (const float*)d_in[12];
-  const float* penb   = (const float*)d_in[14];
-  const float* pelW   = (const float*)d_in[15];
-  const float* pelb   = (const float*)d_in[16];
-  const float* catW   = (const float*)d_in[17];
-  const float* catb   = (const float*)d_in[18];
-  const float* convWg = (const float*)d_in[19];
-  const float* gruWih = (const float*)d_in[20];
-  const float* grubih = (const float*)d_in[21];
-  const float* gruWhh = (const float*)d_in[22];
-  const float* grubhh = (const float*)d_in[23];
-  const float* Wqkv   = (const float*)d_in[24];
-  const float* bqkv   = (const float*)d_in[25];
-  const float* Wo     = (const float*)d_in[26];
-  const float* bo     = (const float*)d_in[27];
-  const float* bng    = (const float*)d_in[28];
-  const float* bnb    = (const float*)d_in[29];
-  const float* W1     = (const float*)d_in[30];
-  const float* b1     = (const float*)d_in[31];
-  const float* W2     = (const float*)d_in[32];
-  const float* b2     = (const float*)d_in[33];
-  const float* outW   = (const float*)d_in[34];
-  const float* outb   = (const float*)d_in[35];
+  KArgs A;
+  A.x      = (const float*)d_in[0];
+  A.tt     = (const float*)d_in[1];
+  A.freqs  = (const float*)d_in[2];
+  A.fc1W   = (const float*)d_in[3];
+  A.fc1b   = (const float*)d_in[4];
+  A.fc2W   = (const float*)d_in[5];
+  A.fc2b   = (const float*)d_in[6];
+  A.nodeW  = (const float*)d_in[7];
+  A.nodeb  = (const float*)d_in[8];
+  A.tprojW = (const float*)d_in[9];
+  A.tprojb = (const float*)d_in[10];
+  A.tcatW  = (const float*)d_in[11];
+  A.tcatb  = (const float*)d_in[12];
+  A.penb   = (const float*)d_in[14];
+  A.pelW   = (const float*)d_in[15];
+  A.pelb   = (const float*)d_in[16];
+  A.catW   = (const float*)d_in[17];
+  A.catb   = (const float*)d_in[18];
+  A.convWg = (const float*)d_in[19];
+  A.gruWih = (const float*)d_in[20];
+  A.grubih = (const float*)d_in[21];
+  A.gruWhh = (const float*)d_in[22];
+  A.grubhh = (const float*)d_in[23];
+  A.Wqkv   = (const float*)d_in[24];
+  A.bqkv   = (const float*)d_in[25];
+  A.Wo     = (const float*)d_in[26];
+  A.bo     = (const float*)d_in[27];
+  A.bng    = (const float*)d_in[28];
+  A.bnb    = (const float*)d_in[29];
+  A.W1     = (const float*)d_in[30];
+  A.b1     = (const float*)d_in[31];
+  A.W2     = (const float*)d_in[32];
+  A.b2     = (const float*)d_in[33];
+  A.outW   = (const float*)d_in[34];
+  A.outb   = (const float*)d_in[35];
 
   float* ws = (float*)d_ws;
-  float* htime = ws;
-  float* hbuf  = htime + 131072;
-  float* gh    = hbuf + 131072;
-  float* s1    = gh + 393216;
-  float* s2    = s1 + 131072;
-  float* smlp  = s2 + 131072;
-  float* o_out = smlp + 131072;
-  float* hsum  = o_out + 131072;
-  float* bnacc = hsum + 320;
-  unsigned short* Qb = (unsigned short*)(bnacc + 1920);
-  unsigned short* Kb = Qb + 262144;
-  unsigned short* Vt = Kb + 262144;
-  float* h0p  = (float*)(Vt + 65536);
-
-  dim3 Blk(256);
-
-  k_pre<<<dim3(1024), Blk, 0, stream>>>(x, tt, freqs, fc1W, fc1b, fc2W, fc2b,
-                                        tprojW, tprojb, nodeW, h0p, htime, hsum);
-
-  k_assemble<<<dim3(512), Blk, 0, stream>>>(h0p, htime, nodeb, tcatW, tcatb,
-                                            penb, pelW, pelb, catW, catb, hbuf);
-
-  for (int l=0; l<NLAY; ++l){
-    const float* bnaccPrev = (l==0) ? bnacc : bnacc + (l-1)*384;
-    const float* gPrev = (l==0) ? bng : bng + (l-1)*192 + 128;
-    const float* bPrev = (l==0) ? bnb : bnb + (l-1)*192 + 128;
-    k_A<<<dim3(256), Blk, 0, stream>>>(smlp, bnaccPrev, gPrev, bPrev,
-                                       hbuf, hsum + l*64,
-                                       gruWhh + l*12288, grubhh + l*192,
-                                       Wqkv + l*12288, bqkv + l*192,
-                                       gh, Qb, Kb, Vt, (l==0) ? 1 : 0);
-    k_attn<<<dim3(512), Blk, 0, stream>>>(Qb, Kb, Vt, o_out);
-    k_B2<<<dim3(256), Blk, 0, stream>>>(hbuf, gh, hsum + l*64, o_out,
-                                        convWg + l*4096, gruWih + l*12288, grubih + l*192,
-                                        Wo + l*4096, bo + l*64,
-                                        s1, s2, bnacc + l*384);
-    k_C<<<dim3(256), Blk, 0, stream>>>(s1, s2, bng + l*192, bnb + l*192,
-                                       W1 + l*8192, b1 + l*128, W2 + l*8192, b2 + l*64,
-                                       smlp, bnacc + l*384);
-  }
-
-  k_out<<<dim3(512), Blk, 0, stream>>>(smlp, bnacc + 4*384, bng + 896, bnb + 896,
-                                       outW, outb, (float*)d_out);
+  A.htime = ws;
+  A.hbuf  = A.htime + 131072;
+  A.gh    = A.hbuf + 131072;
+  A.s1    = A.gh + 393216;
+  A.s2    = A.s1 + 131072;
+  A.smlp  = A.s2 + 131072;
+  A.o_out = A.smlp + 131072;
+  A.hsum  = A.o_out + 131072;
+  A.bnacc = A.hsum + 320;
+  A.Qb = (unsigned short*)(A.bnacc + 1920);
+  A.Kb = A.Qb + 262144;
+  A.Vt = A.Kb + 262144;
+  A.h0p  = (float*)(A.Vt + 65536);
+  A.bar  = (unsigned*)(A.h0p + 2*(NB*HDM));
+  A.out  = (float*)d_out;
+
+  hipMemsetAsync(A.bar, 0, 64*sizeof(unsigned), stream);
+  k_fused<<<dim3(NBLK), dim3(256), 0, stream>>>(A);
 }
```
